# Performance work log

Measured on AMD Instinct MI355X. Metric: run time of the kernel, lower is better.

## Reference

```python
import jax, jax.numpy as jnp
import numpy as np

N = 100000
C = 256
E = 3200000


def setup_inputs() -> dict:
    key = jax.random.key(0)
    ks = jax.random.split(key, 8)
    x = jax.random.normal(ks[0], (N, C), dtype=jnp.float32)
    edge_index = jax.random.randint(ks[1], (2, E), 0, N, dtype=jnp.int64)
    s = 1.0 / np.sqrt(C)
    W_gcn = jax.random.uniform(ks[2], (C, C), jnp.float32, -s, s)
    b_gcn = jnp.zeros((C,), jnp.float32)
    W1 = jax.random.uniform(ks[3], (C, C), jnp.float32, -s, s)
    b1 = jax.random.uniform(ks[4], (C,), jnp.float32, -s, s)
    W2 = jax.random.uniform(ks[5], (1, C), jnp.float32, -s, s)
    b2 = jax.random.uniform(ks[6], (1,), jnp.float32, -s, s)
    return {"x": x, "edge_index": edge_index, "W_gcn": W_gcn, "b_gcn": b_gcn,
            "W1": W1, "b1": b1, "W2": W2, "b2": b2}


def gcn_conv(x, edge_index, W, b):
    n = x.shape[0]
    # add self loops (PyG default add_self_loops=True)
    loop = jnp.arange(n, dtype=edge_index.dtype)
    row = jnp.concatenate([edge_index[0], loop])  # source j
    col = jnp.concatenate([edge_index[1], loop])  # target i
    # symmetric normalization: deg computed over targets (col)
    deg = jax.ops.segment_sum(jnp.ones_like(col, dtype=x.dtype), col, num_segments=n)
    dinv = jnp.where(deg > 0, jax.lax.rsqrt(deg), 0.0)
    norm = dinv[row] * dinv[col]  # [E+N]
    h = x @ W.T  # [N, C], linear (bias applied after aggregation)
    msg = h[row] * norm[:, None]  # gather + scale
    out = jax.ops.segment_sum(msg, col, num_segments=n)  # scatter-add to targets
    return out + b


def reference(x, edge_index, W_gcn, b_gcn, W1, b1, W2, b2):
    h = jax.nn.relu(gcn_conv(x, edge_index, W_gcn, b_gcn))
    h = jax.nn.relu(h @ W1.T + b1)
    h = jax.nn.relu(h @ W2.T + b2)  # [N, 1]
    return jax.nn.sigmoid(h)
```

## Files before the change

### kernel.cpp

```cpp
#include <hip/hip_runtime.h>
#include <math.h>

#define NN 100000
#define CC 256
#define EE 3200000

#define NBINS 1563
#define NBLK 256
#define EPB 12500
#define CAP 4096

typedef unsigned short u16;
typedef __attribute__((ext_vector_type(4))) float f32x4;
typedef __attribute__((ext_vector_type(8))) short bf16x8;

__device__ __forceinline__ float bf2f(u16 u) {
    return __uint_as_float(((unsigned int)u) << 16);
}
__device__ __forceinline__ u16 f2bf(float f) {
    unsigned int x = __float_as_uint(f);
    unsigned int r = (x + 0x7FFF + ((x >> 16) & 1)) >> 16;
    return (u16)r;
}

#define GLOAD_LDS16(gsrc, ldst)                                                        \
    __builtin_amdgcn_global_load_lds((const __attribute__((address_space(1))) void*)(gsrc), \
                                     (__attribute__((address_space(3))) void*)(ldst), 16, 0, 0)


__global__ __launch_bounds__(256) void k_cvt_q8(const float* __restrict__ in,
                                                const float* __restrict__ dinv,
                                                char* __restrict__ xq,
                                                float* __restrict__ scales) {
    int row = blockIdx.x * 4 + (threadIdx.x >> 6);
    if (row >= NN) return;
    int lane = threadIdx.x & 63;
    float dn = dinv[row];
    float4 v = ((const float4*)(in + (size_t)row * CC))[lane];
    v.x *= dn; v.y *= dn; v.z *= dn; v.w *= dn;
    float m = fmaxf(fmaxf(fabsf(v.x), fabsf(v.y)), fmaxf(fabsf(v.z), fabsf(v.w)));
    #pragma unroll
    for (int off = 1; off < 64; off <<= 1) m = fmaxf(m, __shfl_xor(m, off, 64));
    float inv = (m > 0.f) ? 127.f / m : 0.f;
    float sc  = (m > 0.f) ? m / 127.f : 0.f;
    char4 q;
    q.x = (char)(int)rintf(v.x * inv);
    q.y = (char)(int)rintf(v.y * inv);
    q.z = (char)(int)rintf(v.z * inv);
    q.w = (char)(int)rintf(v.w * inv);
    ((char4*)(xq + (size_t)row * CC))[lane] = q;
    if (lane == 0) scales[row] = sc;
}


__global__ __launch_bounds__(256) void k_zero(int* __restrict__ cnt) {
    int i = blockIdx.x * 256 + threadIdx.x;
    if (i < NN) cnt[i] = 0;
}

__global__ __launch_bounds__(256) void k_count_hist(const int* __restrict__ col,
                                                    int* __restrict__ cnt,
                                                    int* __restrict__ G) {
    __shared__ int hist[NBINS];
    const int tid = threadIdx.x;
    const int b0 = blockIdx.x;
    for (int i = tid; i < NBINS; i += 256) hist[i] = 0;
    __syncthreads();
    const int base = b0 * EPB;
    for (int i = 0; i < (EPB + 255) / 256; ++i) {
        int loc = i * 256 + tid;
        if (loc < EPB) {
            int c = col[base + loc];
            atomicAdd(&cnt[c], 1);
            atomicAdd(&hist[c >> 6], 1);
        }
    }
    __syncthreads();
    for (int i = tid; i < NBINS; i += 256) G[i * NBLK + b0] = hist[i];
}

__global__ __launch_bounds__(256) void k_dinv(const int* __restrict__ cnt,
                                              float* __restrict__ dinv) {
    int i = blockIdx.x * 256 + threadIdx.x;
    if (i < NN) dinv[i] = rsqrtf((float)(cnt[i] + 1));
}


__global__ __launch_bounds__(256) void k_binsum(const int* __restrict__ G,
                                                int* __restrict__ binsum) {
    __shared__ int red[4];
    const int bin = blockIdx.x;
    const int t = threadIdx.x;
    int v = G[bin * NBLK + t];
    #pragma unroll
    for (int off = 32; off >= 1; off >>= 1) v += __shfl_down(v, off, 64);
    if ((t & 63) == 0) red[t >> 6] = v;
    __syncthreads();
    if (t == 0) binsum[bin] = red[0] + red[1] + red[2] + red[3];
}

__global__ __launch_bounds__(1024) void k_scanbins(const int* __restrict__ binsum,
                                                   int* __restrict__ binptr) {
    __shared__ int sums[1024];
    const int t = threadIdx.x;
    const int chunk = (NBINS + 1023) / 1024;
    int beg = t * chunk;
    int end = beg + chunk; if (end > NBINS) end = NBINS;
    int s = 0;
    for (int i = beg; i < end; ++i) s += binsum[i];
    sums[t] = s;
    __syncthreads();
    for (int off = 1; off < 1024; off <<= 1) {
        int v = sums[t];
        int u = (t >= off) ? sums[t - off] : 0;
        __syncthreads();
        sums[t] = v + u;
        __syncthreads();
    }
    int run = (t == 0) ? 0 : sums[t - 1];
    for (int i = beg; i < end; ++i) {
        binptr[i] = run;
        run += binsum[i];
    }
    if (t == 1023) binptr[NBINS] = run;
}

__global__ __launch_bounds__(256) void k_scanrow(int* __restrict__ G,
                                                 const int* __restrict__ binptr) {
    __shared__ int buf[256];
    const int bin = blockIdx.x;
    const int t = threadIdx.x;
    int v = G[bin * NBLK + t];
    buf[t] = v;
    __syncthreads();
    for (int off = 1; off < 256; off <<= 1) {
        int u = (t >= off) ? buf[t - off] : 0;
        __syncthreads();
        buf[t] += u;
        __syncthreads();
    }
    G[bin * NBLK + t] = binptr[bin] + buf[t] - v;
}

__global__ __launch_bounds__(256) void k_binscatter(const int* __restrict__ rowi,
                                                    const int* __restrict__ coli,
                                                    const int* __restrict__ G,
                                                    int* __restrict__ binned) {
    __shared__ int cursor[NBINS];
    const int tid = threadIdx.x;
    const int b0 = blockIdx.x;
    for (int i = tid; i < NBINS; i += 256) cursor[i] = G[i * NBLK + b0];
    __syncthreads();
    const int base = b0 * EPB;
    for (int i = 0; i < (EPB + 255) / 256; ++i) {
        int loc = i * 256 + tid;
        if (loc < EPB) {
            int e = base + loc;
            int src = rowi[e];
            int c = coli[e];
            int pos = atomicAdd(&cursor[c >> 6], 1);
            binned[pos] = (src << 6) | (c & 63);
        }
    }
}


__global__ __launch_bounds__(256) void k_gather_bins(const int* __restrict__ binptr,
                                                     const int* __restrict__ binned,
                                                     const float* __restrict__ dinv,
                                                     const char* __restrict__ xq,
                                                     const float* __restrict__ scales,
                                                     u16* __restrict__ aggx) {
    __shared__ int sorted[CAP];
    __shared__ int cur64[64];
    __shared__ int ofs[65];
    const int tid = threadIdx.x;
    const int b = blockIdx.x;
    const int beg = binptr[b];
    int num = binptr[b + 1] - beg;
    if (num > CAP) num = CAP;

    if (tid < 64) cur64[tid] = 0;
    __syncthreads();
    for (int i = tid; i < num; i += 256) atomicAdd(&cur64[binned[beg + i] & 63], 1);
    __syncthreads();
    if (tid == 0) {
        int run = 0;
        for (int j = 0; j < 64; ++j) {
            int v = cur64[j];
            ofs[j] = run;
            cur64[j] = run;
            run += v;
        }
        ofs[64] = run;
    }
    __syncthreads();
    for (int i = tid; i < num; i += 256) {
        int p = binned[beg + i];
        int pos = atomicAdd(&cur64[p & 63], 1);
        sorted[pos] = p >> 6;
    }
    __syncthreads();

    const int lane = tid & 63;
    const int wave = tid >> 6;
    #pragma unroll 1
    for (int k = 0; k < 16; ++k) {
        int nl = wave * 16 + k;
        int node = b * 64 + nl;
        if (node >= NN) continue;
        char4 sq = ((const char4*)(xq + (size_t)node * CC))[lane];
        float ssc = scales[node];
        float ax = ssc * (float)sq.x, ay = ssc * (float)sq.y,
              az = ssc * (float)sq.z, aw = ssc * (float)sq.w;

        int jb = ofs[nl], je = ofs[nl + 1];
        int j = jb;
        for (; j + 4 <= je; j += 4) {
            int s0 = sorted[j], s1 = sorted[j + 1], s2 = sorted[j + 2], s3 = sorted[j + 3];
            float c0 = scales[s0], c1 = scales[s1], c2 = scales[s2], c3 = scales[s3];
            char4 a0 = ((const char4*)(xq + (size_t)s0 * CC))[lane];
            char4 a1 = ((const char4*)(xq + (size_t)s1 * CC))[lane];
            char4 a2 = ((const char4*)(xq + (size_t)s2 * CC))[lane];
            char4 a3 = ((const char4*)(xq + (size_t)s3 * CC))[lane];
            ax = fmaf(c0, (float)a0.x, ax); ay = fmaf(c0, (float)a0.y, ay);
            az = fmaf(c0, (float)a0.z, az); aw = fmaf(c0, (float)a0.w, aw);
            ax = fmaf(c1, (float)a1.x, ax); ay = fmaf(c1, (float)a1.y, ay);
            az = fmaf(c1, (float)a1.z, az); aw = fmaf(c1, (float)a1.w, aw);
            ax = fmaf(c2, (float)a2.x, ax); ay = fmaf(c2, (float)a2.y, ay);
            az = fmaf(c2, (float)a2.z, az); aw = fmaf(c2, (float)a2.w, aw);
            ax = fmaf(c3, (float)a3.x, ax); ay = fmaf(c3, (float)a3.y, ay);
            az = fmaf(c3, (float)a3.z, az); aw = fmaf(c3, (float)a3.w, aw);
        }
        for (; j < je; ++j) {
            int s0 = sorted[j];
            float c0 = scales[s0];
            char4 a0 = ((const char4*)(xq + (size_t)s0 * CC))[lane];
            ax = fmaf(c0, (float)a0.x, ax); ay = fmaf(c0, (float)a0.y, ay);
            az = fmaf(c0, (float)a0.z, az); aw = fmaf(c0, (float)a0.w, aw);
        }

        float dn = dinv[node];
        ushort4 o;
        o.x = f2bf(ax * dn); o.y = f2bf(ay * dn);
        o.z = f2bf(az * dn); o.w = f2bf(aw * dn);
        ((ushort4*)(aggx + (size_t)node * CC))[lane] = o;
    }
}


__global__ __launch_bounds__(256) void k_cvt(const float* __restrict__ in,
                                             u16* __restrict__ out, int n4) {
    int i = blockIdx.x * 256 + threadIdx.x;
    if (i >= n4) return;
    float4 v = ((const float4*)in)[i];
    ushort4 o;
    o.x = f2bf(v.x); o.y = f2bf(v.y); o.z = f2bf(v.z); o.w = f2bf(v.w);
    ((ushort4*)out)[i] = o;
}


__global__ __launch_bounds__(256) void k_mlp(const u16* __restrict__ aggx,
                                             const u16* __restrict__ Wg,
                                             const u16* __restrict__ W1b,
                                             const float* __restrict__ b_gcn,
                                             const float* __restrict__ b1,
                                             const float* __restrict__ W2,
                                             const float* __restrict__ b2,
                                             float* __restrict__ out, int M) {
    __shared__ __align__(16) char lds[53504];
    u16* As   = (u16*)lds;
    u16* Bs   = (u16*)(lds + 4096);
    u16* H1   = (u16*)(lds + 20480);
    float* zb = (float*)(lds + 53248);
    const int tid = threadIdx.x;
    const int lane = tid & 63;
    const int wc = tid >> 6;
    const int bm = blockIdx.x * 64;

    if (tid < 64) zb[tid] = 0.f;

    f32x4 acc[4][4] = {};
    for (int k0 = 0; k0 < 256; k0 += 32) {
        {
            int g = tid;
            int row = g >> 2;
            int lc = (g & 3) ^ ((row >> 1) & 3);
            int ga = bm + row; if (ga >= M) ga = M - 1;
            GLOAD_LDS16(aggx + (size_t)ga * 256 + k0 + lc * 8, (char*)As + g * 16);
        }
        #pragma unroll
        for (int i = 0; i < 4; ++i) {
            int g = tid + i * 256;
            int row = g >> 2;
            int lc = (g & 3) ^ ((row >> 1) & 3);
            GLOAD_LDS16(Wg + (size_t)row * 256 + k0 + lc * 8, (char*)Bs + g * 16);
        }
        __syncthreads();
        bf16x8 af[4], bfr[4];
        #pragma unroll
        for (int m = 0; m < 4; ++m) {
            int r = m * 16 + (lane & 15);
            int ch = (lane >> 4) ^ ((r >> 1) & 3);
            af[m] = *(const bf16x8*)&As[r * 32 + ch * 8];
        }
        #pragma unroll
        for (int n = 0; n < 4; ++n) {
            int r = wc * 64 + n * 16 + (lane & 15);
            int ch = (lane >> 4) ^ ((r >> 1) & 3);
            bfr[n] = *(const bf16x8*)&Bs[r * 32 + ch * 8];
        }
        #pragma unroll
        for (int m = 0; m < 4; ++m)
            #pragma unroll
            for (int n = 0; n < 4; ++n)
                acc[m][n] = __builtin_amdgcn_mfma_f32_16x16x32_bf16(af[m], bfr[n],
                                                                    acc[m][n], 0, 0, 0);
        __syncthreads();
    }

    #pragma unroll
    for (int n = 0; n < 4; ++n) {
        int col = wc * 64 + n * 16 + (lane & 15);
        float bv = b_gcn[col];
        #pragma unroll
        for (int m = 0; m < 4; ++m) {
            #pragma unroll
            for (int j = 0; j < 4; ++j) {
                int row = m * 16 + (lane >> 4) * 4 + j;
                float v = fmaxf(acc[m][n][j] + bv, 0.f);
                int ch = (col >> 3) ^ (row & 7);
                H1[row * 256 + ch * 8 + (col & 7)] = f2bf(v);
            }
        }
    }
    __syncthreads();

    f32x4 acc2[4][4] = {};
    for (int k0 = 0; k0 < 256; k0 += 32) {
        #pragma unroll
        for (int i = 0; i < 4; ++i) {
            int g = tid + i * 256;
            int row = g >> 2;
            int lc = (g & 3) ^ ((row >> 1) & 3);
            GLOAD_LDS16(W1b + (size_t)row * 256 + k0 + lc * 8, (char*)Bs + g * 16);
        }
        __syncthreads();
        bf16x8 af[4], bfr[4];
        const int ksc = k0 >> 3;
        #pragma unroll
        for (int m = 0; m < 4; ++m) {
            int r = m * 16 + (lane & 15);
            int ch = (ksc + (lane >> 4)) ^ (r & 7);
            af[m] = *(const bf16x8*)&H1[r * 256 + ch * 8];
        }
        #pragma unroll
        for (int n = 0; n < 4; ++n) {
            int r = wc * 64 + n * 16 + (lane & 15);
            int ch = (lane >> 4) ^ ((r >> 1) & 3);
            bfr[n] = *(const bf16x8*)&Bs[r * 32 + ch * 8];
        }
        #pragma unroll
        for (int m = 0; m < 4; ++m)
            #pragma unroll
            for (int n = 0; n < 4; ++n)
                acc2[m][n] = __builtin_amdgcn_mfma_f32_16x16x32_bf16(af[m], bfr[n],
                                                                     acc2[m][n], 0, 0, 0);
        __syncthreads();
    }

    float w2v[4], b1v[4];
    #pragma unroll
    for (int n = 0; n < 4; ++n) {
        int col = wc * 64 + n * 16 + (lane & 15);
        w2v[n] = W2[col];
        b1v[n] = b1[col];
    }
    #pragma unroll
    for (int m = 0; m < 4; ++m) {
        #pragma unroll
        for (int j = 0; j < 4; ++j) {
            float s = 0.f;
            #pragma unroll
            for (int n = 0; n < 4; ++n) {
                float v = fmaxf(acc2[m][n][j] + b1v[n], 0.f);
                s = fmaf(v, w2v[n], s);
            }
            s += __shfl_xor(s, 1, 64);
            s += __shfl_xor(s, 2, 64);
            s += __shfl_xor(s, 4, 64);
            s += __shfl_xor(s, 8, 64);
            if ((lane & 15) == 0) atomicAdd(&zb[m * 16 + (lane >> 4) * 4 + j], s);
        }
    }
    __syncthreads();
    if (tid < 64) {
        int grow = bm + tid;
        if (grow < M) {
            float z = fmaxf(zb[tid] + b2[0], 0.f);
            out[grow] = 1.0f / (1.0f + expf(-z));
        }
    }
}


extern "C" void kernel_launch(void* const* d_in, const int* in_sizes, int n_in,
                              void* d_out, int out_size, void* d_ws, size_t ws_size,
                              hipStream_t stream) {
    const float* x     = (const float*)d_in[0];
    const int*   eidx  = (const int*)d_in[1];
    const float* W_gcn = (const float*)d_in[2];
    const float* b_gcn = (const float*)d_in[3];
    const float* W1    = (const float*)d_in[4];
    const float* b1    = (const float*)d_in[5];
    const float* W2    = (const float*)d_in[6];
    const float* b2    = (const float*)d_in[7];
    float* out = (float*)d_out;

    const int* e_row = eidx;
    const int* e_col = eidx + EE;

    char* ws = (char*)d_ws;
    const size_t MB = 1024 * 1024;
    float* dinv   = (float*)(ws + 0);
    int*   cnt    = (int*)  (ws + 1 * MB);
    int*   G      = (int*)  (ws + 2 * MB);
    int*   binptr = (int*)  (ws + 4 * MB);
    int*   binsum = (int*)  (ws + 4 * MB + 64 * 1024);
    float* scales = (float*)(ws + 4 * MB + 128 * 1024);
    int*   binned = (int*)  (ws + 5 * MB);
    u16*   WgB    = (u16*)  (ws + 18 * MB);
    u16*   W1B    = (u16*)  (ws + 18 * MB + 256 * 1024);
    char*  xq     = (char*) (ws + 19 * MB);
    u16*   aggx   = (u16*)  (ws + 45 * MB);
    const size_t need = 97 * MB;
    if (ws_size < need) return;

    k_zero<<<(NN + 255) / 256, 256, 0, stream>>>(cnt);
    k_count_hist<<<NBLK, 256, 0, stream>>>(e_col, cnt, G);
    k_dinv<<<(NN + 255) / 256, 256, 0, stream>>>(cnt, dinv);
    k_binsum<<<NBINS, 256, 0, stream>>>(G, binsum);
    k_scanbins<<<1, 1024, 0, stream>>>(binsum, binptr);
    k_scanrow<<<NBINS, 256, 0, stream>>>(G, binptr);
    k_binscatter<<<NBLK, 256, 0, stream>>>(e_row, e_col, G, binned);

    k_cvt_q8<<<(NN + 3) / 4, 256, 0, stream>>>(x, dinv, xq, scales);
    k_cvt<<<(CC * CC / 4 + 255) / 256, 256, 0, stream>>>(W_gcn, WgB, CC * CC / 4);
    k_cvt<<<(CC * CC / 4 + 255) / 256, 256, 0, stream>>>(W1, W1B, CC * CC / 4);

    k_gather_bins<<<NBINS, 256, 0, stream>>>(binptr, binned, dinv, xq, scales, aggx);

    k_mlp<<<NBINS, 256, 0, stream>>>(aggx, WgB, W1B, b_gcn, b1, W2, b2, out, NN);
}
```

Before: 557.3 us.

## Fuse bin gather with MLP and compute degrees from binned edges

```diff
diff --git a/kernel.cpp b/kernel.cpp
--- a/kernel.cpp
+++ b/kernel.cpp
@@ -53,13 +53,7 @@
 }
 
 
-__global__ __launch_bounds__(256) void k_zero(int* __restrict__ cnt) {
-    int i = blockIdx.x * 256 + threadIdx.x;
-    if (i < NN) cnt[i] = 0;
-}
-
 __global__ __launch_bounds__(256) void k_count_hist(const int* __restrict__ col,
-                                                    int* __restrict__ cnt,
                                                     int* __restrict__ G) {
     __shared__ int hist[NBINS];
     const int tid = threadIdx.x;
@@ -69,11 +63,7 @@
     const int base = b0 * EPB;
     for (int i = 0; i < (EPB + 255) / 256; ++i) {
         int loc = i * 256 + tid;
-        if (loc < EPB) {
-            int c = col[base + loc];
-            atomicAdd(&cnt[c], 1);
-            atomicAdd(&hist[c >> 6], 1);
-        }
+        if (loc < EPB) atomicAdd(&hist[col[base + loc] >> 6], 1);
     }
     __syncthreads();
     for (int i = tid; i < NBINS; i += 256) G[i * NBLK + b0] = hist[i];
@@ -165,24 +155,72 @@
 }
 
 
-__global__ __launch_bounds__(256) void k_gather_bins(const int* __restrict__ binptr,
-                                                     const int* __restrict__ binned,
-                                                     const float* __restrict__ dinv,
-                                                     const char* __restrict__ xq,
-                                                     const float* __restrict__ scales,
-                                                     u16* __restrict__ aggx) {
-    __shared__ int sorted[CAP];
-    __shared__ int cur64[64];
-    __shared__ int ofs[65];
+__global__ __launch_bounds__(256) void k_degcnt(const int* __restrict__ binptr,
+                                                const int* __restrict__ binned,
+                                                int* __restrict__ cnt) {
+    __shared__ int h[64];
     const int tid = threadIdx.x;
     const int b = blockIdx.x;
     const int beg = binptr[b];
+    const int num = binptr[b + 1] - beg;
+    if (tid < 64) h[tid] = 0;
+    __syncthreads();
+    for (int i = tid; i < num; i += 256) atomicAdd(&h[binned[beg + i] & 63], 1);
+    __syncthreads();
+    if (tid < 64) {
+        int node = b * 64 + tid;
+        if (node < NN) cnt[node] = h[tid];
+    }
+}
+
+
+__global__ __launch_bounds__(256) void k_cvt(const float* __restrict__ in,
+                                             u16* __restrict__ out, int n4) {
+    int i = blockIdx.x * 256 + threadIdx.x;
+    if (i >= n4) return;
+    float4 v = ((const float4*)in)[i];
+    ushort4 o;
+    o.x = f2bf(v.x); o.y = f2bf(v.y); o.z = f2bf(v.z); o.w = f2bf(v.w);
+    ((ushort4*)out)[i] = o;
+}
+
+
+__global__ __launch_bounds__(256) void k_fused(const int* __restrict__ binptr,
+                                               const int* __restrict__ binned,
+                                               const int* __restrict__ cnt,
+                                               const float* __restrict__ dinv,
+                                               const char* __restrict__ xq,
+                                               const float* __restrict__ scales,
+                                               const u16* __restrict__ Wg,
+                                               const u16* __restrict__ W1b,
+                                               const float* __restrict__ b_gcn,
+                                               const float* __restrict__ b1,
+                                               const float* __restrict__ W2,
+                                               const float* __restrict__ b2,
+                                               float* __restrict__ out, int M) {
+    __shared__ __align__(16) char lds[66560];
+    u16*   AGG    = (u16*)lds;
+    u16*   H1     = (u16*)lds;
+    float* zb     = (float*)(lds + 32768);
+    u16*   Bs     = (u16*)(lds + 33024);
+    int*   sorted = (int*)(lds + 49408);
+    int*   cur64  = (int*)(lds + 65792);
+    int*   ofs    = (int*)(lds + 66048);
+
+    const int tid = threadIdx.x;
+    const int lane = tid & 63;
+    const int wave = tid >> 6;
+    const int b = blockIdx.x;
+    const int bm = b * 64;
+    const int beg = binptr[b];
     int num = binptr[b + 1] - beg;
     if (num > CAP) num = CAP;
 
-    if (tid < 64) cur64[tid] = 0;
-    __syncthreads();
-    for (int i = tid; i < num; i += 256) atomicAdd(&cur64[binned[beg + i] & 63], 1);
+    if (tid < 64) {
+        zb[tid] = 0.f;
+        int node = bm + tid;
+        cur64[tid] = (node < M) ? cnt[node] : 0;
+    }
     __syncthreads();
     if (tid == 0) {
         int run = 0;
@@ -198,23 +236,23 @@
     for (int i = tid; i < num; i += 256) {
         int p = binned[beg + i];
         int pos = atomicAdd(&cur64[p & 63], 1);
-        sorted[pos] = p >> 6;
-    }
-    __syncthreads();
-
-    const int lane = tid & 63;
-    const int wave = tid >> 6;
+        if (pos < CAP) sorted[pos] = p >> 6;
+    }
+    __syncthreads();
+
     #pragma unroll 1
     for (int k = 0; k < 16; ++k) {
         int nl = wave * 16 + k;
-        int node = b * 64 + nl;
-        if (node >= NN) continue;
+        int node = bm + nl;
+        if (node >= M) continue;
         char4 sq = ((const char4*)(xq + (size_t)node * CC))[lane];
         float ssc = scales[node];
         float ax = ssc * (float)sq.x, ay = ssc * (float)sq.y,
               az = ssc * (float)sq.z, aw = ssc * (float)sq.w;
 
         int jb = ofs[nl], je = ofs[nl + 1];
+        if (jb > CAP) jb = CAP;
+        if (je > CAP) je = CAP;
         int j = jb;
         for (; j + 4 <= je; j += 4) {
             int s0 = sorted[j], s1 = sorted[j + 1], s2 = sorted[j + 2], s3 = sorted[j + 3];
@@ -244,51 +282,13 @@
         ushort4 o;
         o.x = f2bf(ax * dn); o.y = f2bf(ay * dn);
         o.z = f2bf(az * dn); o.w = f2bf(aw * dn);
-        ((ushort4*)(aggx + (size_t)node * CC))[lane] = o;
-    }
-}
-
-
-__global__ __launch_bounds__(256) void k_cvt(const float* __restrict__ in,
-                                             u16* __restrict__ out, int n4) {
-    int i = blockIdx.x * 256 + threadIdx.x;
-    if (i >= n4) return;
-    float4 v = ((const float4*)in)[i];
-    ushort4 o;
-    o.x = f2bf(v.x); o.y = f2bf(v.y); o.z = f2bf(v.z); o.w = f2bf(v.w);
-    ((ushort4*)out)[i] = o;
-}
-
-
-__global__ __launch_bounds__(256) void k_mlp(const u16* __restrict__ aggx,
-                                             const u16* __restrict__ Wg,
-                                             const u16* __restrict__ W1b,
-                                             const float* __restrict__ b_gcn,
-                                             const float* __restrict__ b1,
-                                             const float* __restrict__ W2,
-                                             const float* __restrict__ b2,
-                                             float* __restrict__ out, int M) {
-    __shared__ __align__(16) char lds[53504];
-    u16* As   = (u16*)lds;
-    u16* Bs   = (u16*)(lds + 4096);
-    u16* H1   = (u16*)(lds + 20480);
-    float* zb = (float*)(lds + 53248);
-    const int tid = threadIdx.x;
-    const int lane = tid & 63;
-    const int wc = tid >> 6;
-    const int bm = blockIdx.x * 64;
-
-    if (tid < 64) zb[tid] = 0.f;
+        int byteoff = nl * 512 + (((lane >> 1) ^ ((nl >> 1) & 3)) << 4) + ((lane & 1) << 3);
+        *(ushort4*)((char*)AGG + byteoff) = o;
+    }
+    __syncthreads();
 
     f32x4 acc[4][4] = {};
     for (int k0 = 0; k0 < 256; k0 += 32) {
-        {
-            int g = tid;
-            int row = g >> 2;
-            int lc = (g & 3) ^ ((row >> 1) & 3);
-            int ga = bm + row; if (ga >= M) ga = M - 1;
-            GLOAD_LDS16(aggx + (size_t)ga * 256 + k0 + lc * 8, (char*)As + g * 16);
-        }
         #pragma unroll
         for (int i = 0; i < 4; ++i) {
             int g = tid + i * 256;
@@ -298,15 +298,16 @@
         }
         __syncthreads();
         bf16x8 af[4], bfr[4];
+        const int cb = k0 >> 3;
         #pragma unroll
         for (int m = 0; m < 4; ++m) {
             int r = m * 16 + (lane & 15);
-            int ch = (lane >> 4) ^ ((r >> 1) & 3);
-            af[m] = *(const bf16x8*)&As[r * 32 + ch * 8];
+            int ch = cb + ((lane >> 4) ^ ((r >> 1) & 3));
+            af[m] = *(const bf16x8*)&AGG[r * 256 + ch * 8];
         }
         #pragma unroll
         for (int n = 0; n < 4; ++n) {
-            int r = wc * 64 + n * 16 + (lane & 15);
+            int r = wave * 64 + n * 16 + (lane & 15);
             int ch = (lane >> 4) ^ ((r >> 1) & 3);
             bfr[n] = *(const bf16x8*)&Bs[r * 32 + ch * 8];
         }
@@ -321,7 +322,7 @@
 
     #pragma unroll
     for (int n = 0; n < 4; ++n) {
-        int col = wc * 64 + n * 16 + (lane & 15);
+        int col = wave * 64 + n * 16 + (lane & 15);
         float bv = b_gcn[col];
         #pragma unroll
         for (int m = 0; m < 4; ++m) {
@@ -356,7 +357,7 @@
         }
         #pragma unroll
         for (int n = 0; n < 4; ++n) {
-            int r = wc * 64 + n * 16 + (lane & 15);
+            int r = wave * 64 + n * 16 + (lane & 15);
             int ch = (lane >> 4) ^ ((r >> 1) & 3);
             bfr[n] = *(const bf16x8*)&Bs[r * 32 + ch * 8];
         }
@@ -372,7 +373,7 @@
     float w2v[4], b1v[4];
     #pragma unroll
     for (int n = 0; n < 4; ++n) {
-        int col = wc * 64 + n * 16 + (lane & 15);
+        int col = wave * 64 + n * 16 + (lane & 15);
         w2v[n] = W2[col];
         b1v[n] = b1[col];
     }
@@ -432,23 +433,21 @@
     u16*   WgB    = (u16*)  (ws + 18 * MB);
     u16*   W1B    = (u16*)  (ws + 18 * MB + 256 * 1024);
     char*  xq     = (char*) (ws + 19 * MB);
-    u16*   aggx   = (u16*)  (ws + 45 * MB);
-    const size_t need = 97 * MB;
+    const size_t need = 45 * MB;
     if (ws_size < need) return;
 
-    k_zero<<<(NN + 255) / 256, 256, 0, stream>>>(cnt);
-    k_count_hist<<<NBLK, 256, 0, stream>>>(e_col, cnt, G);
-    k_dinv<<<(NN + 255) / 256, 256, 0, stream>>>(cnt, dinv);
+    k_count_hist<<<NBLK, 256, 0, stream>>>(e_col, G);
     k_binsum<<<NBINS, 256, 0, stream>>>(G, binsum);
     k_scanbins<<<1, 1024, 0, stream>>>(binsum, binptr);
     k_scanrow<<<NBINS, 256, 0, stream>>>(G, binptr);
     k_binscatter<<<NBLK, 256, 0, stream>>>(e_row, e_col, G, binned);
+    k_degcnt<<<NBINS, 256, 0, stream>>>(binptr, binned, cnt);
+    k_dinv<<<(NN + 255) / 256, 256, 0, stream>>>(cnt, dinv);
 
     k_cvt_q8<<<(NN + 3) / 4, 256, 0, stream>>>(x, dinv, xq, scales);
     k_cvt<<<(CC * CC / 4 + 255) / 256, 256, 0, stream>>>(W_gcn, WgB, CC * CC / 4);
     k_cvt<<<(CC * CC / 4 + 255) / 256, 256, 0, stream>>>(W1, W1B, CC * CC / 4);
 
-    k_gather_bins<<<NBINS, 256, 0, stream>>>(binptr, binned, dinv, xq, scales, aggx);
-
-    k_mlp<<<NBINS, 256, 0, stream>>>(aggx, WgB, W1B, b_gcn, b1, W2, b2, out, NN);
-}
+    k_fused<<<NBINS, 256, 0, stream>>>(binptr, binned, cnt, dinv, xq, scales,
+                                       WgB, W1B, b_gcn, b1, W2, b2, out, NN);
+}
```

New measurement: 631.2 us. 1.13x slower.
